# Kernel optimization log

Measured on AMD Instinct MI355X. Metric: run time of the kernel, lower is better.

Reference implementation:

```python
import jax, jax.numpy as jnp
import numpy as np

D = 512      # latent channels (d)
K = 512      # codebook size (k)
PATCH = 8    # encoder conv kernel/stride


def _nearest_embed(z, W):
    """z: (B, D, H, W) latents; W: (D, K) codebook. Returns (quantized (B,D,H,W), argmin (B,H,W))."""
    B, d, H, Wd = z.shape
    zf = z.transpose(0, 2, 3, 1).reshape(-1, d)                      # (N, D)
    # squared L2 distances to each code: ||z||^2 - 2 z.W + ||e||^2
    d2 = (jnp.sum(zf * zf, axis=1, keepdims=True)
          - 2.0 * (zf @ W)
          + jnp.sum(W * W, axis=0))                                   # (N, K)
    idx = jnp.argmin(d2, axis=1)                                      # (N,)
    q = jnp.take(W.T, idx, axis=0)                                    # gather: (N, D)
    q = q.reshape(B, H, Wd, d).transpose(0, 3, 1, 2)
    return q, idx.reshape(B, H, Wd)


def _encode(x, enc_w, enc_b):
    z = jax.lax.conv_general_dilated(x, enc_w, window_strides=(PATCH, PATCH),
                                     padding='VALID',
                                     dimension_numbers=('NCHW', 'OIHW', 'NCHW'))
    return z + enc_b[None, :, None, None]


def _decode(z, dec_w, dec_b):
    y = jax.lax.conv_transpose(z, dec_w, strides=(PATCH, PATCH), padding='VALID',
                               dimension_numbers=('NCHW', 'IOHW', 'NCHW'))
    return y + dec_b[None, :, None, None]


def setup_inputs() -> dict:
    key = jax.random.key(0)
    k1, k2, k3, k4 = jax.random.split(key, 4)
    x = jax.random.normal(k1, (32, 3, 256, 256), dtype=jnp.float32)
    enc_w = jax.random.normal(k2, (D, 3, PATCH, PATCH), dtype=jnp.float32) * 0.02
    enc_b = jnp.zeros((D,), jnp.float32)
    dec_w = jax.random.normal(k3, (D, 3, PATCH, PATCH), dtype=jnp.float32) * 0.02  # IOHW
    dec_b = jnp.zeros((3,), jnp.float32)
    # embedding.weight.normal_(0, 0.02); torch.fmod(weight, 0.04)
    emb_w = jnp.fmod(jax.random.normal(k4, (D, K), dtype=jnp.float32) * 0.02, 0.04)
    return {"x": x, "enc_w": enc_w, "enc_b": enc_b,
            "dec_w": dec_w, "dec_b": dec_b, "emb_w": emb_w}


def reference(x, enc_w, enc_b, dec_w, dec_b, emb_w):
    z_e = _encode(x, enc_w, enc_b)                                    # (32, 512, 32, 32)
    # lookup 1: weight_sg=True (codebook grad stopped) + straight-through estimator
    q1, argmin = _nearest_embed(z_e, jax.lax.stop_gradient(emb_w))
    z_q = z_e + jax.lax.stop_gradient(q1 - z_e)
    # lookup 2: detached encoder output, grads flow to codebook via scatter-add
    emb, _ = _nearest_embed(jax.lax.stop_gradient(z_e), emb_w)
    recon = _decode(z_q, dec_w, dec_b)                                # (32, 3, 256, 256)
    return recon, z_e, emb, argmin
```

## Files before the change

kernel.cpp:

```cpp
#include <hip/hip_runtime.h>
#include <cfloat>

#define PIXB 1024
static const size_t OFF_Z = 6291456;
static const size_t OFF_E = 23068672;
static const size_t OFF_A = 39845888;

typedef __attribute__((address_space(1))) const unsigned int cg_u32;
typedef __attribute__((address_space(3))) unsigned int l_u32;
typedef _Float16 f16x8 __attribute__((ext_vector_type(8)));
typedef float f32x16 __attribute__((ext_vector_type(16)));

#define SPLIT_SCALE 4096.0f
#define SPLIT_INV   (1.0f / 4096.0f)

#define GL16(srcp, dstp) __builtin_amdgcn_global_load_lds((cg_u32*)(srcp), (l_u32*)(dstp), 16, 0, 0)

__global__ __launch_bounds__(256) void k_prep(const float* __restrict__ W,
                                              const float* __restrict__ dw,
                                              const float* __restrict__ ew,
                                              _Float16* __restrict__ wq,
                                              float* __restrict__ w2,
                                              _Float16* __restrict__ aq,
                                              _Float16* __restrict__ wrow,
                                              _Float16* __restrict__ dwh,
                                              int do_aux) {
  const int t = threadIdx.x;
  const int bx = blockIdx.x;
  __shared__ float T[64][65];
  __shared__ float T2[128][65];
  if (bx < 32) {
    __shared__ float TS[32][260];
    const int cp = bx >> 4, ch = bx & 15;
#pragma unroll
    for (int i = 0; i < 32; ++i)
      TS[i][t] = W[(size_t)(ch * 32 + i) * 512 + cp * 256 + t];
    __syncthreads();
#pragma unroll
    for (int j = 0; j < 4; ++j) {
      const int u = j * 256 + t;
      const int c = u >> 2, slot = u & 3;
      const int se = slot ^ ((c >> 1) & 3);
      f16x8 h, l;
#pragma unroll
      for (int jj = 0; jj < 8; ++jj) {
        const float v = TS[slot * 8 + jj][c];
        const _Float16 hh = (_Float16)v;
        h[jj] = hh;
        l[jj] = (_Float16)((v - (float)hh) * SPLIT_SCALE);
      }
      _Float16* base = wq + cp * 262144 + ch * 16384 + c * 32 + se * 8;
      *(f16x8*)(base) = h;
      *(f16x8*)(base + 8192) = l;
    }
    return;
  }
  if (bx < 34) {
    const int k = (bx - 32) * 256 + t;
    float acc = 0.f;
    for (int d = 0; d < 512; ++d) { const float v = W[(size_t)d * 512 + k]; acc = fmaf(v, v, acc); }
    w2[k] = acc;
    return;
  }
  if (bx < 46) {
    const int ch = bx - 34;
#pragma unroll
    for (int cc = 0; cc < 2; ++cc) {
      const int c = cc * 256 + t;
      const float* src = ew + (size_t)c * 192 + ch * 16;
#pragma unroll
      for (int slot = 0; slot < 2; ++slot) {
        f16x8 h, l;
#pragma unroll
        for (int j = 0; j < 8; ++j) {
          const float v = src[slot * 8 + j];
          const _Float16 hh = (_Float16)v;
          h[j] = hh;
          l[j] = (_Float16)((v - (float)hh) * SPLIT_SCALE);
        }
        const int se = slot ^ ((c >> 2) & 1);
        _Float16* dst = aq + (size_t)ch * 16384 + c * 16 + se * 8;
        *(f16x8*)dst = h;
        *(f16x8*)(dst + 8192) = l;
      }
    }
    return;
  }
  if (!do_aux) return;
  if (bx < 110) {
    const int id = bx - 46;
    const int c0 = (id & 7) * 64, d0 = (id >> 3) * 64;
#pragma unroll
    for (int i = 0; i < 16; ++i) {
      const int dl = i * 4 + (t >> 6);
      T[dl][t & 63] = W[(size_t)(d0 + dl) * 512 + c0 + (t & 63)];
    }
    __syncthreads();
#pragma unroll
    for (int i = 0; i < 16; ++i) {
      const int cl = i * 4 + (t >> 6);
      const int dl = t & 63;
      wrow[(size_t)(c0 + cl) * 512 + d0 + dl] = (_Float16)T[dl][cl];
    }
    return;
  }
  {
    const int id = bx - 110;
    const int m0 = (id % 3) * 64, d0 = (id / 3) * 128;
#pragma unroll
    for (int i = 0; i < 32; ++i) {
      const int idx = i * 256 + t;
      const int dl = idx >> 6, ml = idx & 63;
      T2[dl][ml] = dw[(size_t)(d0 + dl) * 192 + m0 + ml];
    }
    __syncthreads();
#pragma unroll
    for (int i = 0; i < 32; ++i) {
      const int idx = i * 256 + t;
      const int ml = idx >> 7, dl = idx & 127;
      dwh[(size_t)(m0 + ml) * 512 + d0 + dl] = (_Float16)T2[dl][ml];
    }
  }
}

__global__ __launch_bounds__(512) void k_encmfma(const float* __restrict__ x,
                                                 const _Float16* __restrict__ aq,
                                                 const float* __restrict__ eb,
                                                 float* __restrict__ out) {
  __shared__ __align__(16) unsigned char CB[131072];
  __shared__ float ebL[512];
  const int t = threadIdx.x;
  ebL[t] = eb[t];
  const int w = t >> 6, lane = t & 63;
  const int wc = w & 3, wp = w >> 2;
  const int n0 = blockIdx.x * 64;
  const int b = n0 >> 10, pixbase = n0 & 1023;
  const int i0 = pixbase >> 5;
  const int row = lane & 31, hi = lane >> 5;

  int ab[4];
#pragma unroll
  for (int ct = 0; ct < 4; ++ct) {
    const int c = wc * 128 + ct * 32 + row;
    ab[ct] = c * 32 + ((hi ^ ((c >> 2) & 1)) << 4);
  }
  const int u = t & 255, srow = u >> 6, vsl = u & 63;
  const int csrc = vsl ^ ((vsl >> 3) & 1);
  const float* xb = x + ((size_t)b * 3 * 256 + (i0 + (srow >> 1)) * 8 + (srow & 1)) * 256 + csrc * 4;
  const int bv0 = (((2 * row) ^ ((row >> 2) & 1)) << 4);
  const int bv1 = (((2 * row + 1) ^ ((row >> 2) & 1)) << 4);
  const int brb = wp * 4096 + (wp * 2 + hi) * 1024;

  f32x16 accA[4], accB[4];
#pragma unroll
  for (int ct = 0; ct < 4; ++ct) { accA[ct] = (f32x16)(0.0f); accB[ct] = (f32x16)(0.0f); }

#define STAGE_A(chv) { const _Float16* as_ = aq + (size_t)(chv) * 16384 + t * 8;            \
    char* ad_ = (char*)CB + ((chv) % 3) * 32768 + t * 16;                                   \
    GL16(as_, ad_); GL16(as_ + 4096, ad_ + 8192);                                           \
    GL16(as_ + 8192, ad_ + 16384); GL16(as_ + 12288, ad_ + 24576); }
#define STAGE_B(chv) GL16(xb + (((chv) >> 2) * 65536 + ((chv) & 3) * 512),                  \
                          (char*)CB + 98304 + (((chv) & 3)) * 8192 + t * 16)
#define ECOMP(chv)                                                                          \
  { const char* abuf = (const char*)CB + ((chv) % 3) * 32768;                               \
    const char* bbuf = (const char*)CB + 98304 + ((chv) & 3) * 8192 + brb;                  \
    const float4 xa = *(const float4*)(bbuf + bv0);                                         \
    const float4 xc = *(const float4*)(bbuf + bv1);                                         \
    const float xs[8] = {xa.x, xa.y, xa.z, xa.w, xc.x, xc.y, xc.z, xc.w};                   \
    f16x8 Bh, Bl;                                                                           \
    _Pragma("unroll") for (int q = 0; q < 8; ++q) {                                         \
      const _Float16 hh = (_Float16)xs[q];                                                  \
      Bh[q] = hh; Bl[q] = (_Float16)((xs[q] - (float)hh) * SPLIT_SCALE); }                  \
    __builtin_amdgcn_s_setprio(1);                                                          \
    _Pragma("unroll") for (int ct_ = 0; ct_ < 4; ++ct_) {                                   \
      const f16x8 Ah = *(const f16x8*)(abuf + ab[ct_]);                                     \
      const f16x8 Al = *(const f16x8*)(abuf + 16384 + ab[ct_]);                             \
      accA[ct_] = __builtin_amdgcn_mfma_f32_32x32x16_f16(Ah, Bh, accA[ct_], 0, 0, 0);       \
      accB[ct_] = __builtin_amdgcn_mfma_f32_32x32x16_f16(Ah, Bl, accB[ct_], 0, 0, 0);       \
      accB[ct_] = __builtin_amdgcn_mfma_f32_32x32x16_f16(Al, Bh, accB[ct_], 0, 0, 0); }     \
    __builtin_amdgcn_s_setprio(0); }
#define EPHASE(chv, waitlit)                                                                \
  { asm volatile("s_waitcnt vmcnt(" #waitlit ")" ::: "memory");                             \
    __builtin_amdgcn_sched_barrier(0);                                                      \
    __builtin_amdgcn_s_barrier();                                                           \
    ECOMP(chv);                                                                             \
    __builtin_amdgcn_s_barrier(); }

  STAGE_A(0); STAGE_B(0);
  STAGE_A(1); STAGE_B(1);
  STAGE_B(2);
#pragma unroll 1
  for (int ch = 0; ch < 9; ++ch) {
    STAGE_A(ch + 2);
    STAGE_B(ch + 3);
    EPHASE(ch, 11);
  }
  STAGE_A(11);
  EPHASE(9, 10);
  EPHASE(10, 5);
  EPHASE(11, 0);
#undef STAGE_A
#undef STAGE_B
#undef ECOMP
#undef EPHASE

  const int pl = wp * 32 + row;
#pragma unroll
  for (int ct = 0; ct < 4; ++ct) {
#pragma unroll
    for (int r = 0; r < 16; ++r) {
      const int c = wc * 128 + ct * 32 + (r & 3) + ((r >> 2) << 3) + (hi << 2);
      out[OFF_Z + ((size_t)(b * 512 + c)) * 1024 + pixbase + pl] =
          fmaf(accB[ct][r], SPLIT_INV, accA[ct][r]) + ebL[c];
    }
  }
}

__global__ __launch_bounds__(512) void k_dist(const _Float16* __restrict__ wq,
                                              const float* __restrict__ Wc,
                                              const float* __restrict__ w2ws,
                                              float* __restrict__ out) {
  __shared__ __align__(16) unsigned char CB[131072];
  __shared__ float WV[512];
  __shared__ int   WI[512];
  __shared__ int   IDX[64];
  const int t = threadIdx.x;
  const int w = t >> 6, lane = t & 63;
  const int wc = w & 3, wp = w >> 2;
  const int n0 = blockIdx.x * 64;
  const int b = n0 >> 10, pixbase = n0 & 1023;
  const int row = lane & 31, hi = lane >> 5;
  const int pl = wp * 32 + row;

  int abase[2][2];
#pragma unroll
  for (int ct = 0; ct < 2; ++ct) {
    const int cl = wc * 64 + ct * 32 + row;
    const int sw = ((cl >> 1) & 3) << 4;
#pragma unroll
    for (int ks = 0; ks < 2; ++ks)
      abase[ct][ks] = cl * 64 + (((ks << 5) | (hi << 4)) ^ sw);
  }
  const float* zsrc = out + OFF_Z + ((size_t)(b * 512 + (t >> 4))) * 1024 + pixbase + (t & 15) * 4;

#define STAGE_W(cpv, chv)                                                        \
  { const _Float16* ws_ = wq + (cpv) * 262144 + (chv) * 16384 + t * 8;           \
    char* wd_ = (char*)CB + ((chv) % 3) * 32768 + t * 16;                        \
    GL16(ws_, wd_); GL16(ws_ + 4096, wd_ + 8192);                                \
    GL16(ws_ + 8192, wd_ + 16384); GL16(ws_ + 12288, wd_ + 24576); }
#define STAGE_Z(chv)                                                             \
  GL16(zsrc + (size_t)(chv) * 32768,                                             \
       (char*)CB + 98304 + ((chv) & 3) * 8192 + t * 16)
#define COMPUTE(chv)                                                             \
  { const char* wb_ = (const char*)CB + ((chv) % 3) * 32768;                     \
    const char* zb_ = (const char*)CB + 98304 + ((chv) & 3) * 8192;              \
    f16x8 Bh0, Bl0, Bh1, Bl1;                                                    \
    _Pragma("unroll") for (int q = 0; q < 8; ++q) {                              \
      const float f0 = *(const float*)(zb_ + (hi * 8 + q) * 256 + pl * 4);       \
      const _Float16 h0 = (_Float16)f0;                                          \
      Bh0[q] = h0; Bl0[q] = (_Float16)((f0 - (float)h0) * SPLIT_SCALE);          \
      const float f1 = *(const float*)(zb_ + (16 + hi * 8 + q) * 256 + pl * 4);  \
      const _Float16 h1 = (_Float16)f1;                                          \
      Bh1[q] = h1; Bl1[q] = (_Float16)((f1 - (float)h1) * SPLIT_SCALE); }        \
    __builtin_amdgcn_s_setprio(1);                                               \
    _Pragma("unroll")                                                            \
    for (int ct_ = 0; ct_ < 2; ++ct_) {                                          \
      const f16x8 Ah0 = *(const f16x8*)(wb_ + abase[ct_][0]);                    \
      const f16x8 Al0 = *(const f16x8*)(wb_ + 16384 + abase[ct_][0]);            \
      const f16x8 Ah1 = *(const f16x8*)(wb_ + abase[ct_][1]);                    \
      const f16x8 Al1 = *(const f16x8*)(wb_ + 16384 + abase[ct_][1]);            \
      accA[ct_] = __builtin_amdgcn_mfma_f32_32x32x16_f16(Ah0, Bh0, accA[ct_], 0, 0, 0); \
      accB[ct_] = __builtin_amdgcn_mfma_f32_32x32x16_f16(Ah0, Bl0, accB[ct_], 0, 0, 0); \
      accB[ct_] = __builtin_amdgcn_mfma_f32_32x32x16_f16(Al0, Bh0, accB[ct_], 0, 0, 0); \
      accA[ct_] = __builtin_amdgcn_mfma_f32_32x32x16_f16(Ah1, Bh1, accA[ct_], 0, 0, 0); \
      accB[ct_] = __builtin_amdgcn_mfma_f32_32x32x16_f16(Ah1, Bl1, accB[ct_], 0, 0, 0); \
      accB[ct_] = __builtin_amdgcn_mfma_f32_32x32x16_f16(Al1, Bh1, accB[ct_], 0, 0, 0); \
    }                                                                            \
    __builtin_amdgcn_s_setprio(0); }
#define PHASE(chv, waitlit)                                                      \
  { asm volatile("s_waitcnt vmcnt(" #waitlit ")" ::: "memory");                  \
    __builtin_amdgcn_sched_barrier(0);                                           \
    __builtin_amdgcn_s_barrier();                                                \
    COMPUTE(chv);                                                                \
    __builtin_amdgcn_s_barrier(); }

  float bv = FLT_MAX; int bi = 0x7fffffff;

#pragma unroll 1
  for (int cp = 0; cp < 2; ++cp) {
    f32x16 accA[2], accB[2];
#pragma unroll
    for (int ct = 0; ct < 2; ++ct) { accA[ct] = (f32x16)(0.0f); accB[ct] = (f32x16)(0.0f); }
    STAGE_W(cp, 0); STAGE_Z(0);
    STAGE_W(cp, 1); STAGE_Z(1);
    STAGE_Z(2);
#pragma unroll 1
    for (int ch = 0; ch < 13; ++ch) {
      STAGE_W(cp, ch + 2);
      STAGE_Z(ch + 3);
      PHASE(ch, 11);
    }
    STAGE_W(cp, 15);
    PHASE(13, 10);
    PHASE(14, 5);
    PHASE(15, 0);

#pragma unroll
    for (int ct = 0; ct < 2; ++ct) {
#pragma unroll
      for (int r = 0; r < 16; ++r) {
        const int code = cp * 256 + wc * 64 + ct * 32 +
                         ((r & 3) + ((r >> 2) << 3) + (hi << 2));
        const float zw = fmaf(accB[ct][r], SPLIT_INV, accA[ct][r]);
        const float d2 = fmaf(-2.f, zw, w2ws[code]);
        if (d2 < bv || (d2 == bv && code < bi)) { bv = d2; bi = code; }
      }
    }
  }
#undef STAGE_W
#undef STAGE_Z
#undef COMPUTE
#undef PHASE

  WV[w * 64 + lane] = bv;
  WI[w * 64 + lane] = bi;
  __syncthreads();
  if (t < 64) {
    const int pw = t >> 5;
    float fbv = FLT_MAX; int fbi = 0x7fffffff;
#pragma unroll
    for (int wcc = 0; wcc < 4; ++wcc)
#pragma unroll
      for (int hh = 0; hh < 2; ++hh) {
        const int li = (pw * 4 + wcc) * 64 + (t & 31) + hh * 32;
        const float v = WV[li];
        const int ii = WI[li];
        if (v < fbv || (v == fbv && ii < fbi)) { fbv = v; fbi = ii; }
      }
    out[OFF_A + n0 + t] = (float)fbi;
    IDX[t] = fbi;
  }
  __syncthreads();

  const int pix = t & 63;
  const int kidx = IDX[pix];
  for (int d = t >> 6; d < 512; d += 8)
    out[OFF_E + ((size_t)(b * 512 + d)) * 1024 + pixbase + pix] = Wc[(size_t)d * 512 + kidx];
}

__global__ __launch_bounds__(512) void k_decmfma(const _Float16* __restrict__ wrow,
                                                 const _Float16* __restrict__ dwh,
                                                 const float* __restrict__ db,
                                                 float* __restrict__ out) {
  __shared__ __align__(16) _Float16 QB[2][4096];
  __shared__ int KIDX[128];
  const int t = threadIdx.x;
  const int w = t >> 6, lane = t & 63;
  const int pt = w & 3, mg = w >> 2;
  const int blk = blockIdx.x;
  const int b = blk >> 3;
  const int pixbase = (blk & 7) * 128;
  if (t < 128) KIDX[t] = (int)out[OFF_A + b * 1024 + pixbase + t];
  __syncthreads();
  const int pixS = t >> 2, slotS = t & 3;
  const _Float16* qsrc = wrow + (size_t)KIDX[pixS] * 512 + slotS * 8;
  const int ldsW = pixS * 32 + (slotS ^ ((pixS >> 1) & 3)) * 8;

  const _Float16* abp[3];
#pragma unroll
  for (int mt = 0; mt < 3; ++mt)
    abp[mt] = dwh + (size_t)((mg * 3 + mt) * 32 + (lane & 31)) * 512 + ((lane >> 5) << 3);

  const int brow = pt * 32 + (lane & 31);
  const int bsw = (brow >> 1) & 3;
  int boff[2];
#pragma unroll
  for (int ks = 0; ks < 2; ++ks)
    boff[ks] = brow * 32 + (((ks * 2 + (lane >> 5)) ^ bsw)) * 8;

  f32x16 acc[3];
#pragma unroll
  for (int mt = 0; mt < 3; ++mt) acc[mt] = (f32x16)(0.0f);
  f16x8 A[2][3][2];
  f16x8 qd[2];

  qd[0] = *(const f16x8*)(qsrc);
#pragma unroll
  for (int mt = 0; mt < 3; ++mt)
#pragma unroll
    for (int ks = 0; ks < 2; ++ks)
      A[0][mt][ks] = *(const f16x8*)(abp[mt] + ks * 16);
  *(f16x8*)&QB[0][ldsW] = qd[0];
  qd[1] = *(const f16x8*)(qsrc + 32);
  __syncthreads();

#pragma unroll
  for (int ch = 0; ch < 16; ++ch) {
    const int par = ch & 1;
    if (ch < 15) {
      *(f16x8*)&QB[par ^ 1][ldsW] = qd[(ch + 1) & 1];
#pragma unroll
      for (int mt = 0; mt < 3; ++mt)
#pragma unroll
        for (int ks = 0; ks < 2; ++ks)
          A[par ^ 1][mt][ks] = *(const f16x8*)(abp[mt] + (ch + 1) * 32 + ks * 16);
    }
    if (ch < 14) qd[ch & 1] = *(const f16x8*)(qsrc + (ch + 2) * 32);
    const f16x8 B0 = *(const f16x8*)&QB[par][boff[0]];
    const f16x8 B1 = *(const f16x8*)&QB[par][boff[1]];
#pragma unroll
    for (int mt = 0; mt < 3; ++mt) {
      acc[mt] = __builtin_amdgcn_mfma_f32_32x32x16_f16(A[par][mt][0], B0, acc[mt], 0, 0, 0);
      acc[mt] = __builtin_amdgcn_mfma_f32_32x32x16_f16(A[par][mt][1], B1, acc[mt], 0, 0, 0);
    }
    __syncthreads();
  }

  const float b0 = db[0], b1 = db[1], b2 = db[2];
  const int pix = pixbase + pt * 32 + (lane & 31);
  const int i = pix >> 5, j = pix & 31;
#pragma unroll
  for (int mt = 0; mt < 3; ++mt) {
    const int m0 = (mg * 3 + mt) * 32;
#pragma unroll
    for (int r = 0; r < 16; ++r) {
      const int m = m0 + (r & 3) + ((r >> 2) << 3) + ((lane >> 5) << 2);
      const int c = m >> 6, ki = (m >> 3) & 7, kj = m & 7;
      const float bias = (c == 0) ? b0 : ((c == 1) ? b1 : b2);
      out[(((size_t)b * 3 + c) * 256 + i * 8 + 7 - ki) * 256 + j * 8 + 7 - kj] = acc[mt][r] + bias;
    }
  }
}

__global__ __launch_bounds__(256) void k_decode(const float* __restrict__ dw,
                                                const float* __restrict__ db,
                                                float* out) {
  __shared__ __align__(16) float Qs[32][132];
  __shared__ __align__(16) float Ws3[32][68];
  const int n0 = blockIdx.x * 128;
  const int b = n0 / PIXB, pixbase = n0 % PIXB;
  const int mt = blockIdx.y;
  const int t = threadIdx.x;
  const int pg = t & 31, ck = t >> 5;
  float acc[4][8];
#pragma unroll
  for (int p = 0; p < 4; ++p)
#pragma unroll
    for (int k = 0; k < 8; ++k) acc[p][k] = 0.f;
  for (int dc = 0; dc < 16; ++dc) {
#pragma unroll
    for (int ii = 0; ii < 4; ++ii) {
      const int id = t + ii * 256;
      const int dd = id >> 5, p4 = id & 31;
      *reinterpret_cast<float4*>(&Qs[dd][p4 * 4]) =
        *reinterpret_cast<const float4*>(&out[OFF_E + ((size_t)b * 512 + dc * 32 + dd) * 1024 + pixbase + p4 * 4]);
    }
#pragma unroll
    for (int ii = 0; ii < 2; ++ii) {
      const int id = t + ii * 256;
      const int dd = id >> 4, m4 = id & 15;
      *reinterpret_cast<float4*>(&Ws3[dd][m4 * 4]) =
        *reinterpret_cast<const float4*>(&dw[(size_t)(dc * 32 + dd) * 192 + mt * 64 + m4 * 4]);
    }
    __syncthreads();
#pragma unroll
    for (int dd = 0; dd < 32; ++dd) {
      const float4 qv = *reinterpret_cast<const float4*>(&Qs[dd][pg * 4]);
      const float4 wa = *reinterpret_cast<const float4*>(&Ws3[dd][ck * 8]);
      const float4 wb = *reinterpret_cast<const float4*>(&Ws3[dd][ck * 8 + 4]);
      const float q[4] = {qv.x, qv.y, qv.z, qv.w};
      const float wv[8] = {wa.x, wa.y, wa.z, wa.w, wb.x, wb.y, wb.z, wb.w};
#pragma unroll
      for (int p = 0; p < 4; ++p)
#pragma unroll
        for (int k = 0; k < 8; ++k) acc[p][k] = fmaf(q[p], wv[k], acc[p][k]);
    }
    __syncthreads();
  }
  const int ckg = mt * 8 + ck;
  const int c = ckg >> 3, ki = ckg & 7;
  const float bias = db[c];
#pragma unroll
  for (int p = 0; p < 4; ++p) {
    const int pix = pixbase + pg * 4 + p;
    const int i = pix >> 5, j = pix & 31;
    const size_t base = (((size_t)b * 3 + c) * 256 + i * 8 + 7 - ki) * 256 + j * 8;
#pragma unroll
    for (int kj = 0; kj < 8; ++kj) out[base + 7 - kj] = acc[p][kj] + bias;
  }
}

extern "C" void kernel_launch(void* const* d_in, const int* in_sizes, int n_in,
                              void* d_out, int out_size, void* d_ws, size_t ws_size,
                              hipStream_t stream) {
  const float* x     = (const float*)d_in[0];
  const float* enc_w = (const float*)d_in[1];
  const float* enc_b = (const float*)d_in[2];
  const float* dec_w = (const float*)d_in[3];
  const float* dec_b = (const float*)d_in[4];
  const float* emb_w = (const float*)d_in[5];
  float* out = (float*)d_out;
  float* w2 = (float*)d_ws;
  _Float16* wrow = (_Float16*)((char*)d_ws + 2048);
  _Float16* dwh  = (_Float16*)((char*)d_ws + 2048 + 524288);
  const int do_aux = (ws_size >= (size_t)(2048 + 524288 + 196608)) ? 1 : 0;
  _Float16* wq  = (_Float16*)d_out;
  _Float16* aq  = (_Float16*)((char*)d_out + 2097152);

  k_prep<<<122, 256, 0, stream>>>(emb_w, dec_w, enc_w, wq, w2, aq, wrow, dwh, do_aux);
  k_encmfma<<<512, 512, 0, stream>>>(x, aq, enc_b, out);
  k_dist<<<512, 512, 0, stream>>>(wq, emb_w, w2, out);
  if (do_aux)
    k_decmfma<<<256, 512, 0, stream>>>(wrow, dwh, dec_b, out);
  else
    k_decode<<<dim3(256, 3), 256, 0, stream>>>(dec_w, dec_b, out);
}
```

Baseline: 192.8 us.

## Pre-split and transpose z chunk into fp16 hi/lo LDS buffer one stage ahead

Each phase now converts the next z chunk into swizzled fp16 hi/lo tiles in a new double-buffered LDS region. The current chunk's B operands are then read as vector LDS loads instead of 16 scalar loads plus conversions per wave. This moves the split work out of the MFMA critical path and cuts redundant per-wave conversion, since each element is now converted once per block. The cost is 16 KB more LDS per block, extra LDS writes, an lgkmcnt drain before each barrier, and retuned vmcnt waits in the pipeline.

```diff
diff --git a/kernel.cpp b/kernel.cpp
--- a/kernel.cpp
+++ b/kernel.cpp
@@ -9,6 +9,7 @@
 typedef __attribute__((address_space(1))) const unsigned int cg_u32;
 typedef __attribute__((address_space(3))) unsigned int l_u32;
 typedef _Float16 f16x8 __attribute__((ext_vector_type(8)));
+typedef _Float16 f16x4 __attribute__((ext_vector_type(4)));
 typedef float f32x16 __attribute__((ext_vector_type(16)));
 
 #define SPLIT_SCALE 4096.0f
@@ -220,7 +221,7 @@
                                               const float* __restrict__ Wc,
                                               const float* __restrict__ w2ws,
                                               float* __restrict__ out) {
-  __shared__ __align__(16) unsigned char CB[131072];
+  __shared__ __align__(16) unsigned char CB[147456];
   __shared__ float WV[512];
   __shared__ int   WI[512];
   __shared__ int   IDX[64];
@@ -241,6 +242,9 @@
     for (int ks = 0; ks < 2; ++ks)
       abase[ct][ks] = cl * 64 + (((ks << 5) | (hi << 4)) ^ sw);
   }
+  const int bo0 = pl * 64 + (((0 + hi) ^ (pl & 3)) << 4);
+  const int bo1 = pl * 64 + (((2 + hi) ^ (pl & 3)) << 4);
+  const int tw = lane * 64 + ((((w >> 1)) ^ (lane & 3)) << 4) + ((w & 1) << 3);
   const float* zsrc = out + OFF_Z + ((size_t)(b * 512 + (t >> 4))) * 1024 + pixbase + (t & 15) * 4;
 
 #define STAGE_W(cpv, chv)                                                        \
@@ -251,17 +255,24 @@
 #define STAGE_Z(chv)                                                             \
   GL16(zsrc + (size_t)(chv) * 32768,                                             \
        (char*)CB + 98304 + ((chv) & 3) * 8192 + t * 16)
+#define TRANSPOSE(chv)                                                           \
+  { const char* rb_ = (const char*)CB + 98304 + ((chv) & 3) * 8192;              \
+    char* sb_ = (char*)CB + 131072 + ((chv) & 1) * 8192;                         \
+    f16x4 hv_, lv_;                                                              \
+    _Pragma("unroll") for (int j_ = 0; j_ < 4; ++j_) {                           \
+      const float f_ = *(const float*)(rb_ + (4 * w + j_) * 256 + lane * 4);     \
+      const _Float16 hh_ = (_Float16)f_;                                         \
+      hv_[j_] = hh_;                                                             \
+      lv_[j_] = (_Float16)((f_ - (float)hh_) * SPLIT_SCALE); }                   \
+    *(f16x4*)(sb_ + tw) = hv_;                                                   \
+    *(f16x4*)(sb_ + 4096 + tw) = lv_; }
 #define COMPUTE(chv)                                                             \
   { const char* wb_ = (const char*)CB + ((chv) % 3) * 32768;                     \
-    const char* zb_ = (const char*)CB + 98304 + ((chv) & 3) * 8192;              \
-    f16x8 Bh0, Bl0, Bh1, Bl1;                                                    \
-    _Pragma("unroll") for (int q = 0; q < 8; ++q) {                              \
-      const float f0 = *(const float*)(zb_ + (hi * 8 + q) * 256 + pl * 4);       \
-      const _Float16 h0 = (_Float16)f0;                                          \
-      Bh0[q] = h0; Bl0[q] = (_Float16)((f0 - (float)h0) * SPLIT_SCALE);          \
-      const float f1 = *(const float*)(zb_ + (16 + hi * 8 + q) * 256 + pl * 4);  \
-      const _Float16 h1 = (_Float16)f1;                                          \
-      Bh1[q] = h1; Bl1[q] = (_Float16)((f1 - (float)h1) * SPLIT_SCALE); }        \
+    const char* zb_ = (const char*)CB + 131072 + ((chv) & 1) * 8192;             \
+    const f16x8 Bh0 = *(const f16x8*)(zb_ + bo0);                                \
+    const f16x8 Bh1 = *(const f16x8*)(zb_ + bo1);                                \
+    const f16x8 Bl0 = *(const f16x8*)(zb_ + 4096 + bo0);                         \
+    const f16x8 Bl1 = *(const f16x8*)(zb_ + 4096 + bo1);                         \
     __builtin_amdgcn_s_setprio(1);                                               \
     _Pragma("unroll")                                                            \
     for (int ct_ = 0; ct_ < 2; ++ct_) {                                          \
@@ -277,11 +288,23 @@
       accB[ct_] = __builtin_amdgcn_mfma_f32_32x32x16_f16(Al1, Bh1, accB[ct_], 0, 0, 0); \
     }                                                                            \
     __builtin_amdgcn_s_setprio(0); }
-#define PHASE(chv, waitlit)                                                      \
+#define LGKM0                                                                    \
+  { asm volatile("s_waitcnt lgkmcnt(0)" ::: "memory");                           \
+    __builtin_amdgcn_sched_barrier(0); }
+#define PHASE_T(chv, waitlit)                                                    \
+  { asm volatile("s_waitcnt vmcnt(" #waitlit ")" ::: "memory");                  \
+    __builtin_amdgcn_sched_barrier(0);                                           \
+    __builtin_amdgcn_s_barrier();                                                \
+    TRANSPOSE((chv) + 1);                                                        \
+    COMPUTE(chv);                                                                \
+    LGKM0;                                                                       \
+    __builtin_amdgcn_s_barrier(); }
+#define PHASE_F(chv, waitlit)                                                    \
   { asm volatile("s_waitcnt vmcnt(" #waitlit ")" ::: "memory");                  \
     __builtin_amdgcn_sched_barrier(0);                                           \
     __builtin_amdgcn_s_barrier();                                                \
     COMPUTE(chv);                                                                \
+    LGKM0;                                                                       \
     __builtin_amdgcn_s_barrier(); }
 
   float bv = FLT_MAX; int bi = 0x7fffffff;
@@ -294,16 +317,22 @@
     STAGE_W(cp, 0); STAGE_Z(0);
     STAGE_W(cp, 1); STAGE_Z(1);
     STAGE_Z(2);
+    asm volatile("s_waitcnt vmcnt(6)" ::: "memory");
+    __builtin_amdgcn_sched_barrier(0);
+    __builtin_amdgcn_s_barrier();
+    TRANSPOSE(0);
+    LGKM0;
+    __builtin_amdgcn_s_barrier();
 #pragma unroll 1
     for (int ch = 0; ch < 13; ++ch) {
       STAGE_W(cp, ch + 2);
       STAGE_Z(ch + 3);
-      PHASE(ch, 11);
+      PHASE_T(ch, 10);
     }
     STAGE_W(cp, 15);
-    PHASE(13, 10);
-    PHASE(14, 5);
-    PHASE(15, 0);
+    PHASE_T(13, 5);
+    PHASE_T(14, 4);
+    PHASE_F(15, 0);
 
 #pragma unroll
     for (int ct = 0; ct < 2; ++ct) {
@@ -319,8 +348,11 @@
   }
 #undef STAGE_W
 #undef STAGE_Z
+#undef TRANSPOSE
 #undef COMPUTE
-#undef PHASE
+#undef LGKM0
+#undef PHASE_T
+#undef PHASE_F
 
   WV[w * 64 + lane] = bv;
   WI[w * 64 + lane] = bi;
```

Measured after the change: 209.2 us. 8.5% more time.

## Fuse encoder GEMM and codebook distance/argmin into one kernel

Applied to the files above, without the earlier changes.

Merges the encoder MFMA kernel and the distance kernel so each block converts its freshly computed z tile to split fp16 hi/lo in LDS and immediately runs the codebook distance GEMM and argmin. This removes the z round-trip through global memory and a kernel launch. The codebook layout is reordered so it can be read directly from global/L2 without staging. The risk is that codebook loads are no longer pipelined through LDS, and more accumulators may raise register pressure.

```diff
diff --git a/kernel.cpp b/kernel.cpp
--- a/kernel.cpp
+++ b/kernel.cpp
@@ -9,6 +9,7 @@
 typedef __attribute__((address_space(1))) const unsigned int cg_u32;
 typedef __attribute__((address_space(3))) unsigned int l_u32;
 typedef _Float16 f16x8 __attribute__((ext_vector_type(8)));
+typedef _Float16 f16x4 __attribute__((ext_vector_type(4)));
 typedef float f32x16 __attribute__((ext_vector_type(16)));
 
 #define SPLIT_SCALE 4096.0f
@@ -39,19 +40,18 @@
 #pragma unroll
     for (int j = 0; j < 4; ++j) {
       const int u = j * 256 + t;
-      const int c = u >> 2, slot = u & 3;
-      const int se = slot ^ ((c >> 1) & 3);
+      const int cl = u >> 2, kslot = u & 3;
       f16x8 h, l;
 #pragma unroll
       for (int jj = 0; jj < 8; ++jj) {
-        const float v = TS[slot * 8 + jj][c];
+        const float v = TS[kslot * 8 + jj][cl];
         const _Float16 hh = (_Float16)v;
         h[jj] = hh;
         l[jj] = (_Float16)((v - (float)hh) * SPLIT_SCALE);
       }
-      _Float16* base = wq + cp * 262144 + ch * 16384 + c * 32 + se * 8;
+      _Float16* base = wq + ch * 32768 + kslot * 4096 + (cp * 256 + cl) * 8;
       *(f16x8*)(base) = h;
-      *(f16x8*)(base + 8192) = l;
+      *(f16x8*)(base + 16384) = l;
     }
     return;
   }
@@ -123,12 +123,18 @@
   }
 }
 
-__global__ __launch_bounds__(512) void k_encmfma(const float* __restrict__ x,
-                                                 const _Float16* __restrict__ aq,
-                                                 const float* __restrict__ eb,
-                                                 float* __restrict__ out) {
+__global__ __launch_bounds__(512) void k_fused(const float* __restrict__ x,
+                                               const _Float16* __restrict__ aq,
+                                               const _Float16* __restrict__ wq,
+                                               const float* __restrict__ eb,
+                                               const float* __restrict__ w2ws,
+                                               const float* __restrict__ Wc,
+                                               float* __restrict__ out) {
   __shared__ __align__(16) unsigned char CB[131072];
   __shared__ float ebL[512];
+  __shared__ float WV[512];
+  __shared__ int   WI[512];
+  __shared__ int   IDX[64];
   const int t = threadIdx.x;
   ebL[t] = eb[t];
   const int w = t >> 6, lane = t & 63;
@@ -137,6 +143,7 @@
   const int b = n0 >> 10, pixbase = n0 & 1023;
   const int i0 = pixbase >> 5;
   const int row = lane & 31, hi = lane >> 5;
+  const int pl = wp * 32 + row;
 
   int ab[4];
 #pragma unroll
@@ -204,123 +211,72 @@
 #undef ECOMP
 #undef EPHASE
 
-  const int pl = wp * 32 + row;
 #pragma unroll
   for (int ct = 0; ct < 4; ++ct) {
+    float zv[16];
 #pragma unroll
     for (int r = 0; r < 16; ++r) {
       const int c = wc * 128 + ct * 32 + (r & 3) + ((r >> 2) << 3) + (hi << 2);
-      out[OFF_Z + ((size_t)(b * 512 + c)) * 1024 + pixbase + pl] =
-          fmaf(accB[ct][r], SPLIT_INV, accA[ct][r]) + ebL[c];
-    }
-  }
-}
-
-__global__ __launch_bounds__(512) void k_dist(const _Float16* __restrict__ wq,
-                                              const float* __restrict__ Wc,
-                                              const float* __restrict__ w2ws,
-                                              float* __restrict__ out) {
-  __shared__ __align__(16) unsigned char CB[131072];
-  __shared__ float WV[512];
-  __shared__ int   WI[512];
-  __shared__ int   IDX[64];
-  const int t = threadIdx.x;
-  const int w = t >> 6, lane = t & 63;
-  const int wc = w & 3, wp = w >> 2;
-  const int n0 = blockIdx.x * 64;
-  const int b = n0 >> 10, pixbase = n0 & 1023;
-  const int row = lane & 31, hi = lane >> 5;
-  const int pl = wp * 32 + row;
-
-  int abase[2][2];
-#pragma unroll
-  for (int ct = 0; ct < 2; ++ct) {
-    const int cl = wc * 64 + ct * 32 + row;
-    const int sw = ((cl >> 1) & 3) << 4;
-#pragma unroll
-    for (int ks = 0; ks < 2; ++ks)
-      abase[ct][ks] = cl * 64 + (((ks << 5) | (hi << 4)) ^ sw);
-  }
-  const float* zsrc = out + OFF_Z + ((size_t)(b * 512 + (t >> 4))) * 1024 + pixbase + (t & 15) * 4;
-
-#define STAGE_W(cpv, chv)                                                        \
-  { const _Float16* ws_ = wq + (cpv) * 262144 + (chv) * 16384 + t * 8;           \
-    char* wd_ = (char*)CB + ((chv) % 3) * 32768 + t * 16;                        \
-    GL16(ws_, wd_); GL16(ws_ + 4096, wd_ + 8192);                                \
-    GL16(ws_ + 8192, wd_ + 16384); GL16(ws_ + 12288, wd_ + 24576); }
-#define STAGE_Z(chv)                                                             \
-  GL16(zsrc + (size_t)(chv) * 32768,                                             \
-       (char*)CB + 98304 + ((chv) & 3) * 8192 + t * 16)
-#define COMPUTE(chv)                                                             \
-  { const char* wb_ = (const char*)CB + ((chv) % 3) * 32768;                     \
-    const char* zb_ = (const char*)CB + 98304 + ((chv) & 3) * 8192;              \
-    f16x8 Bh0, Bl0, Bh1, Bl1;                                                    \
-    _Pragma("unroll") for (int q = 0; q < 8; ++q) {                              \
-      const float f0 = *(const float*)(zb_ + (hi * 8 + q) * 256 + pl * 4);       \
-      const _Float16 h0 = (_Float16)f0;                                          \
-      Bh0[q] = h0; Bl0[q] = (_Float16)((f0 - (float)h0) * SPLIT_SCALE);          \
-      const float f1 = *(const float*)(zb_ + (16 + hi * 8 + q) * 256 + pl * 4);  \
-      const _Float16 h1 = (_Float16)f1;                                          \
-      Bh1[q] = h1; Bl1[q] = (_Float16)((f1 - (float)h1) * SPLIT_SCALE); }        \
-    __builtin_amdgcn_s_setprio(1);                                               \
-    _Pragma("unroll")                                                            \
-    for (int ct_ = 0; ct_ < 2; ++ct_) {                                          \
-      const f16x8 Ah0 = *(const f16x8*)(wb_ + abase[ct_][0]);                    \
-      const f16x8 Al0 = *(const f16x8*)(wb_ + 16384 + abase[ct_][0]);            \
-      const f16x8 Ah1 = *(const f16x8*)(wb_ + abase[ct_][1]);                    \
-      const f16x8 Al1 = *(const f16x8*)(wb_ + 16384 + abase[ct_][1]);            \
-      accA[ct_] = __builtin_amdgcn_mfma_f32_32x32x16_f16(Ah0, Bh0, accA[ct_], 0, 0, 0); \
-      accB[ct_] = __builtin_amdgcn_mfma_f32_32x32x16_f16(Ah0, Bl0, accB[ct_], 0, 0, 0); \
-      accB[ct_] = __builtin_amdgcn_mfma_f32_32x32x16_f16(Al0, Bh0, accB[ct_], 0, 0, 0); \
-      accA[ct_] = __builtin_amdgcn_mfma_f32_32x32x16_f16(Ah1, Bh1, accA[ct_], 0, 0, 0); \
-      accB[ct_] = __builtin_amdgcn_mfma_f32_32x32x16_f16(Ah1, Bl1, accB[ct_], 0, 0, 0); \
-      accB[ct_] = __builtin_amdgcn_mfma_f32_32x32x16_f16(Al1, Bh1, accB[ct_], 0, 0, 0); \
-    }                                                                            \
-    __builtin_amdgcn_s_setprio(0); }
-#define PHASE(chv, waitlit)                                                      \
-  { asm volatile("s_waitcnt vmcnt(" #waitlit ")" ::: "memory");                  \
-    __builtin_amdgcn_sched_barrier(0);                                           \
-    __builtin_amdgcn_s_barrier();                                                \
-    COMPUTE(chv);                                                                \
-    __builtin_amdgcn_s_barrier(); }
+      zv[r] = fmaf(accB[ct][r], SPLIT_INV, accA[ct][r]) + ebL[c];
+      out[OFF_Z + ((size_t)(b * 512 + c)) * 1024 + pixbase + pl] = zv[r];
+    }
+    const int chz = wc * 4 + ct;
+#pragma unroll
+    for (int ks = 0; ks < 4; ++ks) {
+      f16x4 hv, lv;
+#pragma unroll
+      for (int q = 0; q < 4; ++q) {
+        const float f = zv[ks * 4 + q];
+        const _Float16 hh = (_Float16)f;
+        hv[q] = hh;
+        lv[q] = (_Float16)((f - (float)hh) * SPLIT_SCALE);
+      }
+      char* dst = (char*)CB + chz * 8192 + ks * 1024 + pl * 16 + hi * 8;
+      *(f16x4*)dst = hv;
+      *(f16x4*)(dst + 4096) = lv;
+    }
+  }
+  __syncthreads();
+
+  f32x16 dA[4], dB[4];
+#pragma unroll
+  for (int ct2 = 0; ct2 < 4; ++ct2) { dA[ct2] = (f32x16)(0.0f); dB[ct2] = (f32x16)(0.0f); }
+  const _Float16* wbase = wq + (size_t)(wc * 128 + row) * 8 + hi * 4096;
+
+#pragma unroll
+  for (int ch = 0; ch < 16; ++ch) {
+    const char* zbc = (const char*)CB + ch * 8192;
+    const f16x8 Bh0 = *(const f16x8*)(zbc + hi * 1024 + pl * 16);
+    const f16x8 Bh1 = *(const f16x8*)(zbc + (2 + hi) * 1024 + pl * 16);
+    const f16x8 Bl0 = *(const f16x8*)(zbc + 4096 + hi * 1024 + pl * 16);
+    const f16x8 Bl1 = *(const f16x8*)(zbc + 4096 + (2 + hi) * 1024 + pl * 16);
+#pragma unroll
+    for (int ct2 = 0; ct2 < 4; ++ct2) {
+      const _Float16* wpp = wbase + ch * 32768 + ct2 * 256;
+      const f16x8 Ah0 = *(const f16x8*)(wpp);
+      const f16x8 Ah1 = *(const f16x8*)(wpp + 8192);
+      const f16x8 Al0 = *(const f16x8*)(wpp + 16384);
+      const f16x8 Al1 = *(const f16x8*)(wpp + 24576);
+      dA[ct2] = __builtin_amdgcn_mfma_f32_32x32x16_f16(Ah0, Bh0, dA[ct2], 0, 0, 0);
+      dB[ct2] = __builtin_amdgcn_mfma_f32_32x32x16_f16(Ah0, Bl0, dB[ct2], 0, 0, 0);
+      dB[ct2] = __builtin_amdgcn_mfma_f32_32x32x16_f16(Al0, Bh0, dB[ct2], 0, 0, 0);
+      dA[ct2] = __builtin_amdgcn_mfma_f32_32x32x16_f16(Ah1, Bh1, dA[ct2], 0, 0, 0);
+      dB[ct2] = __builtin_amdgcn_mfma_f32_32x32x16_f16(Ah1, Bl1, dB[ct2], 0, 0, 0);
+      dB[ct2] = __builtin_amdgcn_mfma_f32_32x32x16_f16(Al1, Bh1, dB[ct2], 0, 0, 0);
+    }
+  }
 
   float bv = FLT_MAX; int bi = 0x7fffffff;
-
-#pragma unroll 1
-  for (int cp = 0; cp < 2; ++cp) {
-    f32x16 accA[2], accB[2];
-#pragma unroll
-    for (int ct = 0; ct < 2; ++ct) { accA[ct] = (f32x16)(0.0f); accB[ct] = (f32x16)(0.0f); }
-    STAGE_W(cp, 0); STAGE_Z(0);
-    STAGE_W(cp, 1); STAGE_Z(1);
-    STAGE_Z(2);
-#pragma unroll 1
-    for (int ch = 0; ch < 13; ++ch) {
-      STAGE_W(cp, ch + 2);
-      STAGE_Z(ch + 3);
-      PHASE(ch, 11);
-    }
-    STAGE_W(cp, 15);
-    PHASE(13, 10);
-    PHASE(14, 5);
-    PHASE(15, 0);
-
-#pragma unroll
-    for (int ct = 0; ct < 2; ++ct) {
-#pragma unroll
-      for (int r = 0; r < 16; ++r) {
-        const int code = cp * 256 + wc * 64 + ct * 32 +
-                         ((r & 3) + ((r >> 2) << 3) + (hi << 2));
-        const float zw = fmaf(accB[ct][r], SPLIT_INV, accA[ct][r]);
-        const float d2 = fmaf(-2.f, zw, w2ws[code]);
-        if (d2 < bv || (d2 == bv && code < bi)) { bv = d2; bi = code; }
-      }
-    }
-  }
-#undef STAGE_W
-#undef STAGE_Z
-#undef COMPUTE
-#undef PHASE
+#pragma unroll
+  for (int ct2 = 0; ct2 < 4; ++ct2) {
+#pragma unroll
+    for (int r = 0; r < 16; ++r) {
+      const int code = wc * 128 + ct2 * 32 + ((r & 3) + ((r >> 2) << 3) + (hi << 2));
+      const float zw = fmaf(dB[ct2][r], SPLIT_INV, dA[ct2][r]);
+      const float d2 = fmaf(-2.f, zw, w2ws[code]);
+      if (d2 < bv || (d2 == bv && code < bi)) { bv = d2; bi = code; }
+    }
+  }
 
   WV[w * 64 + lane] = bv;
   WI[w * 64 + lane] = bi;
@@ -508,8 +464,7 @@
   _Float16* aq  = (_Float16*)((char*)d_out + 2097152);
 
   k_prep<<<122, 256, 0, stream>>>(emb_w, dec_w, enc_w, wq, w2, aq, wrow, dwh, do_aux);
-  k_encmfma<<<512, 512, 0, stream>>>(x, aq, enc_b, out);
-  k_dist<<<512, 512, 0, stream>>>(wq, emb_w, w2, out);
+  k_fused<<<512, 512, 0, stream>>>(x, aq, wq, enc_b, w2, emb_w, out);
   if (do_aux)
     k_decmfma<<<256, 512, 0, stream>>>(wrow, dwh, dec_b, out);
   else
```

After: 203.2 us. 5.4% more time.
